# Optimization experiments

Measured on AMD Instinct MI355X. Metric: run time of the kernel, lower is better.

## Reference

```python
import jax, jax.numpy as jnp
import numpy as np
import math


def setup_inputs() -> dict:
    B, L, D, P, V = 4, 4096, 512, 128, 8
    key = jax.random.key(0)
    ki = iter(jax.random.split(key, 40))
    def rn(shape, s=0.02):
        return jax.random.normal(next(ki), shape, jnp.float32) * s
    z = lambda *s: jnp.zeros(s, jnp.float32)
    return dict(
        x=jax.random.normal(next(ki), (B, L, D), jnp.float32),
        W_omega=rn((D, D)), b_omega=z(D),
        omega_scale=jnp.full((D,), 0.01, jnp.float32),
        W_pi1=rn((D, D)), b_pi1=z(D), W_pi2=rn((D, D)), b_pi2=z(D),
        W_m1v=rn((D, D)), b_m1v=z(D),
        W_m1o=rn((D, D)), b_m1o=z(D),
        W_mag=rn((D, D)), b_mag=z(D),
        mag_scale=jnp.asarray(5.0, jnp.float32),
        W_qoff=rn((D, D)), b_qoff=z(D),
        W_kenc=rn((D, P)), b_kenc=z(P),
        W_venc=rn((D, V)), b_venc=z(V),
        W_sk1=rn((2 * D, D)), b_sk1=z(D),
        W_sk2=rn((D, P)), b_sk2=z(P),
        W_sg=rn((D, 1)), b_sg=z(1),
        W_kvo=rn((V, D)), b_kvo=z(D),
        ln_g=jnp.ones((4 * D,), jnp.float32), ln_b=z(4 * D),
        W_o1=rn((4 * D, 2 * D)), b_o1=z(2 * D),
        W_o2=rn((2 * D, D)), b_o2=z(D),
    )


def _lin(h, W, b):
    return h @ W + b


def _gelu(h):
    return jax.nn.gelu(h, approximate=False)  # torch nn.GELU default (erf)


def _forward(x, W_omega, b_omega, omega_scale, W_pi1, b_pi1, W_pi2, b_pi2,
             W_m1v, b_m1v, W_m1o, b_m1o, W_mag, b_mag, mag_scale,
             W_qoff, b_qoff, W_kenc, b_kenc, W_venc, b_venc,
             W_sk1, b_sk1, W_sk2, b_sk2, W_sg, b_sg, W_kvo, b_kvo,
             ln_g, ln_b, W_o1, b_o1, W_o2, b_o2):
    B, L, D = x.shape
    P = W_kenc.shape[1]
    # --- evolving phases ---
    omega_scaled = _lin(x, W_omega, b_omega) * jnp.abs(omega_scale)
    phi_init = _lin(_gelu(_lin(x, W_pi1, b_pi1)), W_pi2, b_pi2)
    phi = phi_init + jnp.cumsum(omega_scaled, axis=1)
    cos_phi, sin_phi = jnp.cos(phi), jnp.sin(phi)
    # --- memory 1: positional phasor memory ---
    v1 = _lin(x, W_m1v, b_m1v)
    magnitude = jax.nn.sigmoid(_lin(x, W_mag, b_mag)) * jnp.abs(mag_scale)
    wv1 = magnitude * v1
    sqrt_mag = jnp.sqrt(jnp.cumsum(magnitude, axis=1) + 1e-8)
    mem1_cos = jnp.cumsum(wv1 * cos_phi, axis=1) / sqrt_mag
    mem1_sin = jnp.cumsum(wv1 * sin_phi, axis=1) / sqrt_mag
    phi_q = phi + _lin(x, W_qoff, b_qoff)
    pos_ret = (mem1_cos * jnp.cos(phi_q) + mem1_sin * jnp.sin(phi_q)) / math.sqrt(D)
    pos_out = _lin(pos_ret, W_m1o, b_m1o)
    # --- memory 2: key/value phasor binding ---
    query_phase = jnp.tanh(_lin(x, W_kenc, b_kenc)) * math.pi
    values = _lin(x, W_venc, b_venc)                      # [B,L,V]
    store_gate = jax.nn.sigmoid(_lin(x, W_sg, b_sg))      # [B,L,1]
    positions = jnp.arange(1, L + 1, dtype=x.dtype)[None, :, None]
    context_avg = jnp.cumsum(x, axis=1) / positions
    sk_in = jnp.concatenate([x, context_avg], axis=-1)
    storage_phase = jnp.tanh(_lin(_gelu(_lin(sk_in, W_sk1, b_sk1)), W_sk2, b_sk2)) * math.pi
    store_cos, store_sin = jnp.cos(storage_phase), jnp.sin(storage_phase)  # [B,L,P]
    gv = values * store_gate                               # [B,L,V]
    # [B,L,P,V] outer products, cumsum along L
    kv_mem_cos = jnp.cumsum(store_cos[..., None] * gv[:, :, None, :], axis=1)
    kv_mem_sin = jnp.cumsum(store_sin[..., None] * gv[:, :, None, :], axis=1)
    gate_cum = jnp.clip(jnp.cumsum(store_gate, axis=1), 1.0, None)  # [B,L,1]
    inv_norm = (1.0 / jnp.sqrt(gate_cum))[..., None]
    kv_mem_cos = kv_mem_cos * inv_norm
    kv_mem_sin = kv_mem_sin * inv_norm
    q_cos, q_sin = jnp.cos(query_phase), jnp.sin(query_phase)
    kv_retrieved = (jnp.einsum('blp,blpv->blv', q_cos, kv_mem_cos)
                    + jnp.einsum('blp,blpv->blv', q_sin, kv_mem_sin)) / math.sqrt(P)
    kv_out = _lin(kv_retrieved, W_kvo, b_kvo)
    # --- output projection ---
    combined = jnp.concatenate([pos_out, kv_out, x * cos_phi, x * sin_phi], axis=-1)
    mu = combined.mean(axis=-1, keepdims=True)
    var = combined.var(axis=-1, keepdims=True)
    h = (combined - mu) / jnp.sqrt(var + 1e-5) * ln_g + ln_b
    h = _gelu(_lin(h, W_o1, b_o1))  # dropout is identity in eval mode
    return x + _lin(h, W_o2, b_o2)


def reference(x, W_omega, b_omega, omega_scale, W_pi1, b_pi1, W_pi2, b_pi2,
              W_m1v, b_m1v, W_m1o, b_m1o, W_mag, b_mag, mag_scale,
              W_qoff, b_qoff, W_kenc, b_kenc, W_venc, b_venc,
              W_sk1, b_sk1, W_sk2, b_sk2, W_sg, b_sg, W_kvo, b_kvo,
              ln_g, ln_b, W_o1, b_o1, W_o2, b_o2):
    return _forward(x, W_omega, b_omega, omega_scale, W_pi1, b_pi1, W_pi2, b_pi2,
                    W_m1v, b_m1v, W_m1o, b_m1o, W_mag, b_mag, mag_scale,
                    W_qoff, b_qoff, W_kenc, b_kenc, W_venc, b_venc,
                    W_sk1, b_sk1, W_sk2, b_sk2, W_sg, b_sg, W_kvo, b_kvo,
                    ln_g, ln_b, W_o1, b_o1, W_o2, b_o2)
```

## Files before the change

kernel.cpp:

```cpp
#include <hip/hip_runtime.h>
#include <math.h>

#define B_ 4
#define L_ 4096
#define D_ 512
#define P_ 128
#define V_ 8
#define N_ (B_*L_)
#define NC 64
#define CL (L_/NC)
#define LD ((size_t)L_*D_)
#define PI_F 3.14159265358979323846f

typedef unsigned short ushort;
typedef __attribute__((ext_vector_type(8))) short bh8;
typedef __attribute__((ext_vector_type(4))) float f4;
typedef const __attribute__((address_space(1))) unsigned int gu32;
typedef __attribute__((address_space(3))) unsigned int lu32;

__device__ __forceinline__ float geluf(float v){
    return 0.5f*v*(1.0f+erff(v*0.7071067811865475f));
}
__device__ __forceinline__ float tanhf_fast(float x){
    return 1.0f - 2.0f/(__expf(2.0f*x)+1.0f);
}
__device__ __forceinline__ ushort f2b(float f){
    union { float f; unsigned u; } v; v.f = f;
    unsigned r = (v.u + 0x7fffu + ((v.u >> 16) & 1u)) >> 16;
    return (ushort)r;
}
__device__ __forceinline__ float b2f(ushort h){
    union { unsigned u; float f; } v; v.u = ((unsigned)h) << 16;
    return v.f;
}
__device__ __forceinline__ void gload16(const ushort* g, ushort* l){
    __builtin_amdgcn_global_load_lds((gu32*)g, (lu32*)l, 16, 0, 0);
}
__device__ __forceinline__ int xcd_swz(int orig, int nwg){
    int q8 = nwg >> 3, r8 = nwg & 7;
    int xcd = orig & 7, sub = orig >> 3;
    return (xcd < r8 ? xcd*(q8+1) : r8*(q8+1) + (xcd-r8)*q8) + sub;
}

template<int ACT>
__global__ __launch_bounds__(256, 2)
void bgemm_k(const ushort* __restrict__ A, int lda,
             const ushort* __restrict__ Wt, const float* __restrict__ bias,
             ushort* __restrict__ Ob0, float* __restrict__ Of,
             int ldc, int K, int M, const float* __restrict__ addbuf)
{
    __shared__ ushort lA[2][128*32];
    __shared__ ushort lB[2][128*32];
    const int tid = threadIdx.x, lane = tid & 63, w = tid >> 6;
    const int wr = w >> 1, wc = w & 1;
    const int nbx = gridDim.x;
    const int wg = xcd_swz(blockIdx.y*nbx + blockIdx.x, nbx*gridDim.y);
    const int row0 = (wg / nbx) * 128, col0 = (wg % nbx) * 128;

    const int srow = w*32 + (lane >> 2);
    const int scol = (lane & 3) * 8;
    const ushort* gA0 = A  + (size_t)(row0 + srow)      * lda + scol;
    const ushort* gA1 = A  + (size_t)(row0 + srow + 16) * lda + scol;
    const ushort* gB0 = Wt + (size_t)(col0 + srow)      * K   + scol;
    const ushort* gB1 = Wt + (size_t)(col0 + srow + 16) * K   + scol;
    const int d0 = srow*32 + scol, d1 = (srow+16)*32 + scol;

    f4 zero4 = {0.f,0.f,0.f,0.f};
    f4 acc[4][4];
    #pragma unroll
    for (int i=0;i<4;i++)
        #pragma unroll
        for (int j=0;j<4;j++) acc[i][j] = zero4;

    const int fr = lane & 15, fq = (lane >> 4) * 8;
    gload16(gA0, &lA[0][d0]); gload16(gA1, &lA[0][d1]);
    gload16(gB0, &lB[0][d0]); gload16(gB1, &lB[0][d1]);
    __syncthreads();
    int cur = 0;
    for (int kt = 0; kt < K; kt += 32) {
        int nxt = cur ^ 1;
        if (kt + 32 < K) {
            gload16(gA0 + kt + 32, &lA[nxt][d0]); gload16(gA1 + kt + 32, &lA[nxt][d1]);
            gload16(gB0 + kt + 32, &lB[nxt][d0]); gload16(gB1 + kt + 32, &lB[nxt][d1]);
        }
        bh8 af[4], bfr[4];
        #pragma unroll
        for (int i=0;i<4;i++){
            af[i]  = *(const bh8*)&lA[cur][(wr*64 + i*16 + fr)*32 + fq];
            bfr[i] = *(const bh8*)&lB[cur][(wc*64 + i*16 + fr)*32 + fq];
        }
        #pragma unroll
        for (int i=0;i<4;i++)
            #pragma unroll
            for (int j=0;j<4;j++)
                acc[i][j] = __builtin_amdgcn_mfma_f32_16x16x32_bf16(af[i], bfr[j], acc[i][j], 0, 0, 0);
        __syncthreads();
        cur = nxt;
    }

    #pragma unroll
    for (int i=0;i<4;i++){
        int rr = row0 + wr*64 + i*16 + ((lane >> 4) << 2);
        #pragma unroll
        for (int j=0;j<4;j++){
            int cc = col0 + wc*64 + j*16 + (lane & 15);
            float bv = bias[cc];
            #pragma unroll
            for (int q=0;q<4;q++){
                int r = rr + q;
                float t = acc[i][j][q] + bv;
                if (ACT==1) t = geluf(t);
                if (addbuf) t += addbuf[(size_t)r*512 + cc];
                if (Of) Of[(size_t)r*ldc + cc] = t;
                else    Ob0[(size_t)r*ldc + cc] = f2b(t);
            }
        }
    }
}

__global__ __launch_bounds__(256, 2)
void fgemm_k(const ushort* __restrict__ A, int lda, const ushort* __restrict__ Wt,
             const float* __restrict__ bs0, const float* __restrict__ bs1,
             const float* __restrict__ bs2, const float* __restrict__ bs3,
             const float* __restrict__ bs4, const float* __restrict__ bs5,
             ushort* __restrict__ o0, ushort* __restrict__ o1p, ushort* __restrict__ o2p,
             ushort* __restrict__ o3p, ushort* __restrict__ o4p,
             ushort* __restrict__ Qc, ushort* __restrict__ Qs,
             const float* __restrict__ omsc, const float* __restrict__ magscp, int K)
{
    __shared__ ushort lA[2][128*32];
    __shared__ ushort lB[2][128*32];
    const int tid = threadIdx.x, lane = tid & 63, w = tid >> 6;
    const int wr = w >> 1, wc = w & 1;
    const int nbx = gridDim.x;
    const int wg = xcd_swz(blockIdx.y*nbx + blockIdx.x, nbx*gridDim.y);
    const int row0 = (wg / nbx) * 128, col0 = (wg % nbx) * 128;

    const int srow = w*32 + (lane >> 2);
    const int scol = (lane & 3) * 8;
    const ushort* gA0 = A  + (size_t)(row0 + srow)      * lda + scol;
    const ushort* gA1 = A  + (size_t)(row0 + srow + 16) * lda + scol;
    const ushort* gB0 = Wt + (size_t)(col0 + srow)      * K   + scol;
    const ushort* gB1 = Wt + (size_t)(col0 + srow + 16) * K   + scol;
    const int d0 = srow*32 + scol, d1 = (srow+16)*32 + scol;

    f4 zero4 = {0.f,0.f,0.f,0.f};
    f4 acc[4][4];
    #pragma unroll
    for (int i=0;i<4;i++)
        #pragma unroll
        for (int j=0;j<4;j++) acc[i][j] = zero4;

    const int fr = lane & 15, fq = (lane >> 4) * 8;
    gload16(gA0, &lA[0][d0]); gload16(gA1, &lA[0][d1]);
    gload16(gB0, &lB[0][d0]); gload16(gB1, &lB[0][d1]);
    __syncthreads();
    int cur = 0;
    for (int kt = 0; kt < K; kt += 32) {
        int nxt = cur ^ 1;
        if (kt + 32 < K) {
            gload16(gA0 + kt + 32, &lA[nxt][d0]); gload16(gA1 + kt + 32, &lA[nxt][d1]);
            gload16(gB0 + kt + 32, &lB[nxt][d0]); gload16(gB1 + kt + 32, &lB[nxt][d1]);
        }
        bh8 af[4], bfr[4];
        #pragma unroll
        for (int i=0;i<4;i++){
            af[i]  = *(const bh8*)&lA[cur][(wr*64 + i*16 + fr)*32 + fq];
            bfr[i] = *(const bh8*)&lB[cur][(wc*64 + i*16 + fr)*32 + fq];
        }
        #pragma unroll
        for (int i=0;i<4;i++)
            #pragma unroll
            for (int j=0;j<4;j++)
                acc[i][j] = __builtin_amdgcn_mfma_f32_16x16x32_bf16(af[i], bfr[j], acc[i][j], 0, 0, 0);
        __syncthreads();
        cur = nxt;
    }

    const int seg = col0 >> 9;
    if (seg == 5) {
        #pragma unroll
        for (int i=0;i<4;i++){
            int rr = row0 + wr*64 + i*16 + ((lane >> 4) << 2);
            #pragma unroll
            for (int j=0;j<4;j++){
                int lcc = (col0 - 2560) + wc*64 + j*16 + (lane & 15);
                float bv = bs5[lcc];
                #pragma unroll
                for (int q=0;q<4;q++){
                    int r = rr + q;
                    float ph = tanhf_fast(acc[i][j][q] + bv)*PI_F;
                    Qc[(size_t)r*128 + lcc] = f2b(__cosf(ph));
                    Qs[(size_t)r*128 + lcc] = f2b(__sinf(ph));
                }
            }
        }
        return;
    }
    const float* bias = seg==0?bs0: seg==1?bs1: seg==2?bs2: seg==3?bs3: bs4;
    ushort* dst = seg==0?o0: seg==1?o1p: seg==2?o2p: seg==3?o3p: o4p;
    float msc = fabsf(*magscp);
    #pragma unroll
    for (int i=0;i<4;i++){
        int rr = row0 + wr*64 + i*16 + ((lane >> 4) << 2);
        #pragma unroll
        for (int j=0;j<4;j++){
            int cc = col0 + wc*64 + j*16 + (lane & 15);
            int lcc = cc & 511;
            float bv = bias[lcc];
            float csc = (seg==0) ? fabsf(omsc[lcc]) : 1.0f;
            #pragma unroll
            for (int q=0;q<4;q++){
                int r = rr + q;
                float t = acc[i][j][q] + bv;
                if (seg==1)      t = msc/(1.0f+__expf(-t));
                else if (seg==3) t = geluf(t);
                else             t *= csc;
                dst[(size_t)r*512 + lcc] = f2b(t);
            }
        }
    }
}

__global__ __launch_bounds__(256, 2)
void mgemm_k(const ushort* __restrict__ Apos, const ushort* __restrict__ Ask,
             const ushort* __restrict__ Wm1o, const ushort* __restrict__ Wsk2,
             const float* __restrict__ bm1o, const float* __restrict__ bsk2,
             ushort* __restrict__ planes, ushort* __restrict__ Kc, ushort* __restrict__ Ks)
{
    __shared__ ushort lA[2][128*32];
    __shared__ ushort lB[2][128*32];
    const int tid = threadIdx.x, lane = tid & 63, w = tid >> 6;
    const int wr = w >> 1, wc = w & 1;
    const int nbx = gridDim.x;
    const int wg = xcd_swz(blockIdx.y*nbx + blockIdx.x, nbx*gridDim.y);
    const int row0 = (wg / nbx) * 128, col0 = (wg % nbx) * 128;
    const int seg = col0 >> 9;
    const ushort* A  = seg ? Ask  : Apos;
    const ushort* Wt = seg ? Wsk2 : Wm1o;
    const int wcol0 = seg ? (col0 - 512) : col0;
    const int K = 512;

    const int srow = w*32 + (lane >> 2);
    const int scol = (lane & 3) * 8;
    const ushort* gA0 = A  + (size_t)(row0 + srow)       * 512 + scol;
    const ushort* gA1 = A  + (size_t)(row0 + srow + 16)  * 512 + scol;
    const ushort* gB0 = Wt + (size_t)(wcol0 + srow)      * 512 + scol;
    const ushort* gB1 = Wt + (size_t)(wcol0 + srow + 16) * 512 + scol;
    const int d0 = srow*32 + scol, d1 = (srow+16)*32 + scol;

    f4 zero4 = {0.f,0.f,0.f,0.f};
    f4 acc[4][4];
    #pragma unroll
    for (int i=0;i<4;i++)
        #pragma unroll
        for (int j=0;j<4;j++) acc[i][j] = zero4;

    const int fr = lane & 15, fq = (lane >> 4) * 8;
    gload16(gA0, &lA[0][d0]); gload16(gA1, &lA[0][d1]);
    gload16(gB0, &lB[0][d0]); gload16(gB1, &lB[0][d1]);
    __syncthreads();
    int cur = 0;
    for (int kt = 0; kt < K; kt += 32) {
        int nxt = cur ^ 1;
        if (kt + 32 < K) {
            gload16(gA0 + kt + 32, &lA[nxt][d0]); gload16(gA1 + kt + 32, &lA[nxt][d1]);
            gload16(gB0 + kt + 32, &lB[nxt][d0]); gload16(gB1 + kt + 32, &lB[nxt][d1]);
        }
        bh8 af[4], bfr[4];
        #pragma unroll
        for (int i=0;i<4;i++){
            af[i]  = *(const bh8*)&lA[cur][(wr*64 + i*16 + fr)*32 + fq];
            bfr[i] = *(const bh8*)&lB[cur][(wc*64 + i*16 + fr)*32 + fq];
        }
        #pragma unroll
        for (int i=0;i<4;i++)
            #pragma unroll
            for (int j=0;j<4;j++)
                acc[i][j] = __builtin_amdgcn_mfma_f32_16x16x32_bf16(af[i], bfr[j], acc[i][j], 0, 0, 0);
        __syncthreads();
        cur = nxt;
    }

    #pragma unroll
    for (int i=0;i<4;i++){
        int rr = row0 + wr*64 + i*16 + ((lane >> 4) << 2);
        #pragma unroll
        for (int j=0;j<4;j++){
            int cc = col0 + wc*64 + j*16 + (lane & 15);
            #pragma unroll
            for (int q=0;q<4;q++){
                int r = rr + q;
                if (seg == 0){
                    planes[(size_t)r*2048 + cc] = f2b(acc[i][j][q] + bm1o[cc]);
                } else {
                    int lcc = cc - 512;
                    float ph = tanhf_fast(acc[i][j][q] + bsk2[lcc])*PI_F;
                    Kc[(size_t)r*128 + lcc] = f2b(__cosf(ph));
                    Ks[(size_t)r*128 + lcc] = f2b(__sinf(ph));
                }
            }
        }
    }
}

__global__ __launch_bounds__(256)
void wtrans_k(const float* __restrict__ W, ushort* __restrict__ Wt, int K, int M)
{
    __shared__ float tile[32][33];
    int kb = blockIdx.y*32, mb = blockIdx.x*32;
    int tx = threadIdx.x & 31, ty = threadIdx.x >> 5;
    #pragma unroll
    for (int i = ty; i < 32; i += 8)
        tile[i][tx] = W[(size_t)(kb+i)*M + mb+tx];
    __syncthreads();
    #pragma unroll
    for (int i = ty; i < 32; i += 8)
        Wt[(size_t)(mb+i)*K + kb+tx] = f2b(tile[tx][i]);
}

__global__ __launch_bounds__(256)
void fconv_k(const float* __restrict__ in, ushort* __restrict__ xctx)
{
    size_t i = ((size_t)blockIdx.x*256 + threadIdx.x) * 4;
    size_t row = i >> 9; int d = (int)(i & 511);
    float4 v = *(const float4*)(in + i);
    ushort* o = xctx + row*1024 + d;
    o[0]=f2b(v.x); o[1]=f2b(v.y); o[2]=f2b(v.z); o[3]=f2b(v.w);
}

__global__ __launch_bounds__(256)
void s1a_k(const ushort* __restrict__ omega, const float* __restrict__ xg,
           float* __restrict__ csA, float* __restrict__ csX)
{
    int bid = blockIdx.x;
    int b = bid >> 7; int rem = bid & 127;
    int dg = rem & 1, c = rem >> 1;
    int d = dg*256 + threadIdx.x;
    size_t base = ((size_t)b*L_ + (size_t)c*CL)*D_ + d;
    float sA=0.f, sX=0.f;
    for (int l=0;l<CL;l++){
        sA += b2f(omega[base + (size_t)l*D_]);
        sX += xg[base + (size_t)l*D_];
    }
    size_t ci = ((size_t)b*NC + c)*D_ + d;
    csA[ci]=sA; csX[ci]=sX;
}

__global__ __launch_bounds__(256)
void aux1_k(float* __restrict__ csA, float* __restrict__ csX,
            const float* __restrict__ sgate, float* __restrict__ rinv, int nb2)
{
    __shared__ float wsum[4];
    __shared__ float carry;
    int bb = blockIdx.x, t = threadIdx.x;
    if (bb < nb2){
        int tt = bb*256 + t;
        int b = tt >> 9, d = tt & 511;
        float* bufs[2] = {csA, csX};
        #pragma unroll
        for (int i=0;i<2;i++){
            float* p = bufs[i] + ((size_t)b*NC)*D_ + d;
            float run=0.f;
            for (int c=0;c<NC;c++){
                float v = p[(size_t)c*D_];
                p[(size_t)c*D_] = run;
                run += v;
            }
        }
        return;
    }
    int b = bb - nb2;
    int lane = t & 63, wave = t >> 6;
    if (t == 0) carry = 0.f;
    __syncthreads();
    for (int s = 0; s < L_/256; s++){
        float v = sgate[(size_t)b*L_ + s*256 + t];
        float sc = v;
        #pragma unroll
        for (int off=1; off<64; off<<=1){
            float u = __shfl_up(sc, off, 64);
            if (lane >= off) sc += u;
        }
        if (lane == 63) wsum[wave] = sc;
        __syncthreads();
        float woff = carry;
        for (int w2 = 0; w2 < wave; w2++) woff += wsum[w2];
        float inc = sc + woff;
        rinv[(size_t)b*L_ + s*256 + t] = rsqrtf(fmaxf(inc, 1.0f));
        __syncthreads();
        if (t == 255) carry = inc;
        __syncthreads();
    }
}

__global__ void prefix_k(float* a, float* b2v, float* c3, int nbuf)
{
    int t = blockIdx.x*blockDim.x + threadIdx.x;
    int b = t >> 9, d = t & 511;
    float* bufs[3] = {a,b2v,c3};
    for (int i=0;i<nbuf;i++){
        float* p = bufs[i] + ((size_t)b*NC)*D_ + d;
        float run=0.f;
        for (int c=0;c<NC;c++){
            float v = p[(size_t)c*D_];
            p[(size_t)c*D_] = run;
            run += v;
        }
    }
}

__global__ __launch_bounds__(256)
void s1c_k(const ushort* __restrict__ omega, const float* __restrict__ xg,
           const ushort* __restrict__ phi_init,
           const ushort* __restrict__ magn, const ushort* __restrict__ v1,
           const float* __restrict__ csA, const float* __restrict__ csX,
           ushort* __restrict__ cphi, ushort* __restrict__ sphi, ushort* __restrict__ xctx,
           float* __restrict__ csM, float* __restrict__ csC, float* __restrict__ csS)
{
    int bid = blockIdx.x;
    int b = bid >> 7; int rem = bid & 127;
    int dg = rem & 1, c = rem >> 1;
    int d = dg*256 + threadIdx.x;
    size_t ci = ((size_t)b*NC + c)*D_ + d;
    float phiacc = csA[ci], xacc = csX[ci];
    float sM=0.f,sC=0.f,sS=0.f;
    size_t xrow = (size_t)b*L_ + (size_t)c*CL;
    size_t base = xrow*D_ + d;
    for (int l=0;l<CL;l++){
        size_t idx = base + (size_t)l*D_;
        phiacc += b2f(omega[idx]);
        float ph = b2f(phi_init[idx]) + phiacc;
        float spv = __sinf(ph), cpv = __cosf(ph);
        cphi[idx] = f2b(cpv); sphi[idx] = f2b(spv);
        xacc += xg[idx];
        xctx[(xrow + l)*1024 + 512 + d] = f2b(__fdividef(xacc, (float)(c*CL + l + 1)));
        float m = b2f(magn[idx]); sM += m;
        float wv = m * b2f(v1[idx]);
        sC = fmaf(wv, cpv, sC); sS = fmaf(wv, spv, sS);
    }
    csM[ci]=sM; csC[ci]=sC; csS[ci]=sS;
}

__global__ __launch_bounds__(256)
void s1e_k(const ushort* __restrict__ magn, const ushort* __restrict__ v1,
           const ushort* qoff, const ushort* __restrict__ cphi, const ushort* __restrict__ sphi,
           const float* __restrict__ csM, const float* __restrict__ csC,
           const float* __restrict__ csS, ushort* pos_ret)
{
    int bid = blockIdx.x;
    int b = bid >> 7; int rem = bid & 127;
    int dg = rem & 1, c = rem >> 1;
    int d = dg*256 + threadIdx.x;
    size_t ci = ((size_t)b*NC + c)*D_ + d;
    float mA=csM[ci], cA=csC[ci], sA=csS[ci];
    size_t base = ((size_t)b*L_ + (size_t)c*CL)*D_ + d;
    for (int l=0;l<CL;l++){
        size_t idx = base + (size_t)l*D_;
        float m = b2f(magn[idx]); mA += m;
        float wv = m * b2f(v1[idx]);
        float cp = b2f(cphi[idx]), sp = b2f(sphi[idx]);
        cA = fmaf(wv, cp, cA); sA = fmaf(wv, sp, sA);
        float rs = rsqrtf(mA + 1e-8f);
        float qo = b2f(qoff[idx]);
        float sq = __sinf(qo), cq = __cosf(qo);
        float cosq = cp*cq - sp*sq;
        float sinq = sp*cq + cp*sq;
        pos_ret[idx] = f2b((cA*cosq + sA*sinq) * rs * 0.04419417382415922f);
    }
}

__global__ __launch_bounds__(256)
void vencsg_k(const float* __restrict__ xg, const float* __restrict__ Wv,
              const float* __restrict__ bv, const float* __restrict__ Wg,
              const float* __restrict__ bg,
              ushort* __restrict__ gvb, float* __restrict__ sgate)
{
    int gw = (int)((blockIdx.x*(size_t)blockDim.x + threadIdx.x) >> 6);
    int lane = threadIdx.x & 63;
    const float* xr = xg + (size_t)gw*D_;
    float pv[8] = {0,0,0,0,0,0,0,0}; float pg = 0.f;
    #pragma unroll
    for (int j=0;j<8;j++){
        int k = lane + 64*j;
        float xv = xr[k];
        #pragma unroll
        for (int v=0;v<8;v++) pv[v] = fmaf(xv, Wv[k*8+v], pv[v]);
        pg = fmaf(xv, Wg[k], pg);
    }
    #pragma unroll
    for (int off=32; off>0; off>>=1){
        #pragma unroll
        for (int v=0;v<8;v++) pv[v] += __shfl_down(pv[v], off, 64);
        pg += __shfl_down(pg, off, 64);
    }
    if (lane==0){
        float sg = 1.0f/(1.0f+__expf(-(pg + bg[0])));
        #pragma unroll
        for (int v=0;v<8;v++) gvb[(size_t)gw*8+v] = f2b((pv[v] + bv[v]) * sg);
        sgate[gw] = sg;
    }
}

__global__ __launch_bounds__(256)
void kvsum_k(const ushort* __restrict__ Kc, const ushort* __restrict__ Ks,
             const ushort* __restrict__ gvb, float* __restrict__ csKV)
{
    int bid = blockIdx.x;
    int b = bid >> 6, c = bid & 63;
    int t = threadIdx.x; int p = t & 127; int v0 = (t>>7)*4;
    size_t row0 = (size_t)b*L_ + (size_t)c*64;
    float ac[4]={0,0,0,0}, as[4]={0,0,0,0};
    for (int l=0;l<64;l++){
        size_t r = row0 + l;
        float kc = b2f(Kc[r*(size_t)P_ + p]);
        float ks = b2f(Ks[r*(size_t)P_ + p]);
        #pragma unroll
        for (int j=0;j<4;j++){
            float gv = b2f(gvb[r*(size_t)V_ + v0 + j]);
            ac[j] = fmaf(kc, gv, ac[j]);
            as[j] = fmaf(ks, gv, as[j]);
        }
    }
    float* base = csKV + ((size_t)b*64 + c)*2048;
    #pragma unroll
    for (int j=0;j<4;j++){
        base[p*V_ + v0 + j] = ac[j];
        base[1024 + p*V_ + v0 + j] = as[j];
    }
}

__global__ void kvpfx_k(float* __restrict__ csKV)
{
    int t = blockIdx.x*blockDim.x + threadIdx.x;
    int b = t >> 11, si = t & 2047;
    float* ptr = csKV + ((size_t)b*64)*2048 + si;
    float run=0.f;
    for (int c=0;c<64;c++){
        float v = ptr[(size_t)c*2048];
        ptr[(size_t)c*2048] = run;
        run += v;
    }
}

__global__ __launch_bounds__(256)
void kv2_k(const ushort* __restrict__ Qc, const ushort* __restrict__ Qs,
           const ushort* __restrict__ Kc, const ushort* __restrict__ Ks,
           const ushort* __restrict__ gvb, const float* __restrict__ rinv,
           const float* __restrict__ csKV, float* __restrict__ kvret)
{
    __shared__ ushort sS[64][66];
    __shared__ float sM[2048];
    __shared__ float sgv[64][8];
    int tile = blockIdx.x, b = blockIdx.y;
    int t = threadIdx.x, lane = t & 63, w = t >> 6;
    int wr = w >> 1, wc = w & 1;
    size_t row0 = (size_t)b*L_ + (size_t)tile*64;
    const float* kvb = csKV + ((size_t)b*64 + tile)*2048;
    #pragma unroll
    for (int k=0;k<8;k++) sM[t + k*256] = kvb[t + k*256];
    #pragma unroll
    for (int k=0;k<2;k++){
        int idx = t + k*256; int l = idx >> 3, v = idx & 7;
        sgv[l][v] = b2f(gvb[(row0 + l)*(size_t)V_ + v]);
    }
    f4 zero4 = {0.f,0.f,0.f,0.f};
    f4 acc[2][2];
    #pragma unroll
    for (int i=0;i<2;i++)
        #pragma unroll
        for (int j=0;j<2;j++) acc[i][j] = zero4;
    #pragma unroll
    for (int ks=0; ks<8; ks++){
        const ushort* Ab = (ks<4) ? Qc : Qs;
        const ushort* Bb = (ks<4) ? Kc : Ks;
        int kb = (ks&3)*32 + (lane>>4)*8;
        bh8 af[2], bfr[2];
        #pragma unroll
        for (int i=0;i<2;i++)
            af[i] = *(const bh8*)(Ab + (row0 + wr*32 + i*16 + (lane&15))*(size_t)P_ + kb);
        #pragma unroll
        for (int j=0;j<2;j++)
            bfr[j] = *(const bh8*)(Bb + (row0 + wc*32 + j*16 + (lane&15))*(size_t)P_ + kb);
        #pragma unroll
        for (int i=0;i<2;i++)
            #pragma unroll
            for (int j=0;j<2;j++)
                acc[i][j] = __builtin_amdgcn_mfma_f32_16x16x32_bf16(af[i], bfr[j], acc[i][j], 0, 0, 0);
    }
    #pragma unroll
    for (int i=0;i<2;i++){
        #pragma unroll
        for (int j=0;j<2;j++){
            int cc = wc*32 + j*16 + (lane & 15);
            #pragma unroll
            for (int q=0;q<4;q++){
                int lr = wr*32 + i*16 + ((lane>>4)<<2) + q;
                sS[lr][cc] = f2b((cc <= lr) ? acc[i][j][q] : 0.f);
            }
        }
    }
    __syncthreads();
    int l = t & 63, vh = t >> 6; int v0 = vh*2;
    const ushort* qcr = Qc + (row0 + l)*(size_t)P_;
    const ushort* qsr = Qs + (row0 + l)*(size_t)P_;
    float a0=0.f, a1=0.f;
    #pragma unroll
    for (int pc=0; pc<16; pc++){
        bh8 qc8 = *(const bh8*)(qcr + pc*8);
        bh8 qs8 = *(const bh8*)(qsr + pc*8);
        #pragma unroll
        for (int e=0;e<8;e++){
            int p = pc*8+e;
            float qc = b2f((ushort)qc8[e]), qs = b2f((ushort)qs8[e]);
            a0 += qc*sM[p*8+v0]   + qs*sM[1024+p*8+v0];
            a1 += qc*sM[p*8+v0+1] + qs*sM[1024+p*8+v0+1];
        }
    }
    for (int c=0;c<64;c++){
        float sv = b2f(sS[l][c]);
        a0 = fmaf(sv, sgv[c][v0],   a0);
        a1 = fmaf(sv, sgv[c][v0+1], a1);
    }
    float rn = rinv[row0 + l] * 0.08838834764831845f;
    kvret[(row0+l)*(size_t)V_ + v0]   = a0*rn;
    kvret[(row0+l)*(size_t)V_ + v0+1] = a1*rn;
}

__global__ __launch_bounds__(256)
void kvo_k(const float* __restrict__ kvret, const float* __restrict__ Wkvo,
           const float* __restrict__ bkvo, ushort* __restrict__ pl)
{
    size_t idx = (size_t)blockIdx.x*256 + threadIdx.x;
    size_t n = idx >> 9; int d = (int)(idx & 511);
    float s = bkvo[d];
    #pragma unroll
    for (int v=0;v<8;v++) s = fmaf(kvret[n*8+v], Wkvo[v*512 + d], s);
    pl[n*2048 + 512 + d] = f2b(s);
}

__global__ __launch_bounds__(256)
void cmb_k(const float* __restrict__ xg, const ushort* __restrict__ cphi,
           const ushort* __restrict__ sphi,
           const float* __restrict__ ln_g, const float* __restrict__ ln_b,
           ushort* pl)
{
    __shared__ float red[8];
    int n = blockIdx.x; int t = threadIdx.x;
    int wave = t>>6, lane = t&63;
    float v_[8]; float sum=0.f, sumsq=0.f;
    #pragma unroll
    for (int i=0;i<8;i++){
        int cidx = t + i*256;
        int seg = cidx >> 9, cc = cidx & 511;
        float v;
        if (seg <= 1) v = b2f(pl[(size_t)n*2048 + cidx]);
        else {
            size_t id = (size_t)n*D_ + cc;
            v = xg[id] * b2f((seg==2) ? cphi[id] : sphi[id]);
        }
        v_[i]=v; sum += v; sumsq = fmaf(v,v,sumsq);
    }
    #pragma unroll
    for (int off=32; off>0; off>>=1){
        sum += __shfl_xor(sum, off, 64);
        sumsq += __shfl_xor(sumsq, off, 64);
    }
    if (lane==0){ red[wave]=sum; red[wave+4]=sumsq; }
    __syncthreads();
    float s = red[0]+red[1]+red[2]+red[3];
    float q = red[4]+red[5]+red[6]+red[7];
    float mu = s * (1.0f/2048.0f);
    float var = q * (1.0f/2048.0f) - mu*mu;
    float rstd = rsqrtf(var + 1e-5f);
    #pragma unroll
    for (int i=0;i<8;i++){
        int cidx = t + i*256;
        float h = (v_[i]-mu)*rstd*ln_g[cidx] + ln_b[cidx];
        pl[(size_t)n*2048 + cidx] = f2b(h);
    }
}

__global__ void copyx_k(const float* __restrict__ x, float* __restrict__ out, size_t n)
{
    size_t i = (size_t)blockIdx.x*256 + threadIdx.x;
    if (i < n) out[i] = x[i];
}

struct WS {
    ushort *wt_fused,*wt_pi2,*wt_sk1,*wt_sk2,*wt_m1o,*wt_o1,*wt_o2;
    ushort *xctx, *pool;
    ushort *Qc,*Qs,*Kc,*Ks,*gvb,*cphi,*sphi;
    float *sgate,*rinv,*kvret;
    float *csA,*csX,*csM,*csC,*csS,*csKV;
};

static size_t ws_layout(WS& w, char* base, int NB)
{
    size_t off = 0;
    auto al = [&](size_t bytes)->char* {
        char* p = base + off; off = (off + bytes + 255) & ~(size_t)255; return p;
    };
    size_t R = (size_t)NB * L_;
    w.wt_fused=(ushort*)al((size_t)2688*512*2);
    w.wt_pi2 =(ushort*)al(512*512*2);
    w.wt_sk1 =(ushort*)al((size_t)512*1024*2); w.wt_sk2=(ushort*)al(128*512*2);
    w.wt_m1o =(ushort*)al(512*512*2);
    w.wt_o1  =(ushort*)al((size_t)1024*2048*2); w.wt_o2=(ushort*)al((size_t)512*1024*2);
    w.xctx=(ushort*)al(R*1024*2);
    w.pool=(ushort*)al(R*512*2*6);
    w.Qc=(ushort*)al(R*128*2); w.Qs=(ushort*)al(R*128*2);
    w.Kc=(ushort*)al(R*128*2); w.Ks=(ushort*)al(R*128*2);
    w.gvb=(ushort*)al(R*8*2);
    w.cphi=(ushort*)al(R*512*2); w.sphi=(ushort*)al(R*512*2);
    w.sgate=(float*)al(R*4); w.rinv=(float*)al(R*4); w.kvret=(float*)al(R*8*4);
    w.csA=(float*)al((size_t)NB*NC*512*4); w.csX=(float*)al((size_t)NB*NC*512*4);
    w.csM=(float*)al((size_t)NB*NC*512*4); w.csC=(float*)al((size_t)NB*NC*512*4);
    w.csS=(float*)al((size_t)NB*NC*512*4);
    w.csKV=(float*)al((size_t)NB*64*2048*4);
    return off;
}

extern "C" void kernel_launch(void* const* d_in, const int* in_sizes, int n_in,
                              void* d_out, int out_size, void* d_ws, size_t ws_size,
                              hipStream_t stream)
{
    const float* x        =(const float*)d_in[0];
    const float* W_omega  =(const float*)d_in[1];  const float* b_omega=(const float*)d_in[2];
    const float* omega_sc =(const float*)d_in[3];
    const float* W_pi1    =(const float*)d_in[4];  const float* b_pi1 =(const float*)d_in[5];
    const float* W_pi2    =(const float*)d_in[6];  const float* b_pi2 =(const float*)d_in[7];
    const float* W_m1v    =(const float*)d_in[8];  const float* b_m1v =(const float*)d_in[9];
    const float* W_m1o    =(const float*)d_in[10]; const float* b_m1o =(const float*)d_in[11];
    const float* W_mag    =(const float*)d_in[12]; const float* b_mag =(const float*)d_in[13];
    const float* mag_sc   =(const float*)d_in[14];
    const float* W_qoff   =(const float*)d_in[15]; const float* b_qoff=(const float*)d_in[16];
    const float* W_kenc   =(const float*)d_in[17]; const float* b_kenc=(const float*)d_in[18];
    const float* W_venc   =(const float*)d_in[19]; const float* b_venc=(const float*)d_in[20];
    const float* W_sk1    =(const float*)d_in[21]; const float* b_sk1 =(const float*)d_in[22];
    const float* W_sk2    =(const float*)d_in[23]; const float* b_sk2 =(const float*)d_in[24];
    const float* W_sg     =(const float*)d_in[25]; const float* b_sg  =(const float*)d_in[26];
    const float* W_kvo    =(const float*)d_in[27]; const float* b_kvo =(const float*)d_in[28];
    const float* ln_g     =(const float*)d_in[29]; const float* ln_b  =(const float*)d_in[30];
    const float* W_o1     =(const float*)d_in[31]; const float* b_o1  =(const float*)d_in[32];
    const float* W_o2     =(const float*)d_in[33]; const float* b_o2  =(const float*)d_in[34];
    float* out = (float*)d_out;

    char* wsb = (char*)d_ws;
    WS w;
    int NB = 4;
    if (ws_layout(w, wsb, 4) > ws_size) {
        NB = 2;
        if (ws_layout(w, wsb, 2) > ws_size) {
            NB = 1;
            if (ws_layout(w, wsb, 1) > ws_size) {
                copyx_k<<<dim3((unsigned)(((size_t)N_*D_ + 255)/256)), dim3(256), 0, stream>>>(x, out, (size_t)N_*D_);
                return;
            }
        }
    }

    dim3 blk(256);
    auto wt = [&](const float* W, ushort* Wt, int K, int M){
        wtrans_k<<<dim3(M/32, K/32), blk, 0, stream>>>(W, Wt, K, M);
    };
    wt(W_omega, w.wt_fused + (size_t)0*512*512, 512, 512);
    wt(W_mag,   w.wt_fused + (size_t)1*512*512, 512, 512);
    wt(W_m1v,   w.wt_fused + (size_t)2*512*512, 512, 512);
    wt(W_pi1,   w.wt_fused + (size_t)3*512*512, 512, 512);
    wt(W_qoff,  w.wt_fused + (size_t)4*512*512, 512, 512);
    wt(W_kenc,  w.wt_fused + (size_t)5*512*512, 512, 128);
    wt(W_pi2,w.wt_pi2,512,512);
    wt(W_sk1,w.wt_sk1,1024,512);  wt(W_sk2,w.wt_sk2,512,128);
    wt(W_m1o,w.wt_m1o,512,512);
    wt(W_o1,w.wt_o1,2048,1024);   wt(W_o2,w.wt_o2,1024,512);

    const int R = NB * L_;
    const size_t SL = (size_t)R * 512;
    ushort* bA = w.pool;        ushort* bB = w.pool + SL;
    ushort* bC = w.pool + 2*SL; ushort* bD = w.pool + 3*SL;
    ushort* bE = w.pool + 4*SL; ushort* bF = w.pool + 5*SL;
    ushort* planes = w.pool;
    ushort* h1 = w.pool + 4*SL;

    #define GEMM(ACT,A,lda,Wt_,bias_,Ob0_,Of_,ldc,K_,M_,add_) \
        bgemm_k<ACT><<<dim3((M_)/128, R/128), blk, 0, stream>>>(A,lda,Wt_,bias_,Ob0_,Of_,ldc,K_,M_,add_)

    for (int g = 0; g < B_/NB; ++g) {
        const float* xg = x + (size_t)g*NB*LD;
        float* outg = out + (size_t)g*NB*LD;

        fconv_k<<<dim3((unsigned)((size_t)R*512/1024)), blk, 0, stream>>>(xg, w.xctx);

        fgemm_k<<<dim3(2688/128, R/128), blk, 0, stream>>>(
            w.xctx,1024, w.wt_fused, b_omega,b_mag,b_m1v,b_pi1,b_qoff,b_kenc,
            bA,bB,bC,bD,bF, w.Qc,w.Qs, omega_sc, mag_sc, 512);
        GEMM(0, bD,512, w.wt_pi2, b_pi2, bE,(float*)0, 512, 512,512, (const float*)0);
        vencsg_k<<<dim3((unsigned)((size_t)R*64/256)), blk, 0, stream>>>(xg, W_venc,b_venc, W_sg,b_sg, w.gvb, w.sgate);
        s1a_k<<<dim3(NB*NC*2), blk, 0, stream>>>(bA, xg, w.csA, w.csX);
        aux1_k<<<dim3(NB*2 + NB), blk, 0, stream>>>(w.csA, w.csX, w.sgate, w.rinv, NB*2);
        s1c_k<<<dim3(NB*NC*2), blk, 0, stream>>>(bA, xg, bE, bB, bC, w.csA, w.csX,
                                                 w.cphi, w.sphi, w.xctx, w.csM, w.csC, w.csS);
        prefix_k<<<dim3(NB*2), blk, 0, stream>>>(w.csM, w.csC, w.csS, 3);
        s1e_k<<<dim3(NB*NC*2), blk, 0, stream>>>(bB, bC, bF, w.cphi, w.sphi,
                                                 w.csM, w.csC, w.csS, bF);

        GEMM(1, w.xctx,1024, w.wt_sk1, b_sk1, bD,(float*)0, 512, 1024,512, (const float*)0);
        mgemm_k<<<dim3(640/128, R/128), blk, 0, stream>>>(
            bF, bD, w.wt_m1o, w.wt_sk2, b_m1o, b_sk2, planes, w.Kc, w.Ks);

        kvsum_k<<<dim3(NB*64), blk, 0, stream>>>(w.Kc, w.Ks, w.gvb, w.csKV);
        kvpfx_k<<<dim3(NB*8), blk, 0, stream>>>(w.csKV);
        kv2_k<<<dim3(64, NB), blk, 0, stream>>>(w.Qc, w.Qs, w.Kc, w.Ks, w.gvb, w.rinv, w.csKV, w.kvret);
        kvo_k<<<dim3((unsigned)((size_t)R*512/256)), blk, 0, stream>>>(w.kvret, W_kvo, b_kvo, planes);

        cmb_k<<<dim3(R), blk, 0, stream>>>(xg, w.cphi, w.sphi, ln_g, ln_b, planes);
        GEMM(1, planes,2048, w.wt_o1, b_o1, h1,(float*)0, 1024, 2048,1024, (const float*)0);
        GEMM(0, h1,1024, w.wt_o2, b_o2, (ushort*)0,outg, 512, 1024,512, xg);
    }
    #undef GEMM
}
```

Before: 541.0 us.

## Replace generic GEMM with 256x128 tile, K=64 swizzled-LDS pipelined kernel

Swaps the 128x128, K-step-32 bf16 GEMM for a 512-thread kernel that computes 256x128 output tiles with a K-step of 64. LDS is XOR-swizzled to avoid bank conflicts, and global-to-LDS loads are overlapped with explicit vmcnt waits and raw s_barrier. The larger tile and deeper K step are meant to raise arithmetic intensity and cut barrier overhead per MFMA. In exchange it uses more LDS, allows one block per CU, and launches fewer workgroups.

```diff
diff --git a/kernel.cpp b/kernel.cpp
--- a/kernel.cpp
+++ b/kernel.cpp
@@ -43,27 +43,25 @@
 }
 
 template<int ACT>
-__global__ __launch_bounds__(256, 2)
-void bgemm_k(const ushort* __restrict__ A, int lda,
+__global__ __launch_bounds__(512, 1)
+void cgemm_k(const ushort* __restrict__ A, int lda,
              const ushort* __restrict__ Wt, const float* __restrict__ bias,
-             ushort* __restrict__ Ob0, float* __restrict__ Of,
-             int ldc, int K, int M, const float* __restrict__ addbuf)
-{
-    __shared__ ushort lA[2][128*32];
-    __shared__ ushort lB[2][128*32];
+             ushort* __restrict__ Ob, float* __restrict__ Of,
+             int ldc, int K, const float* __restrict__ addbuf)
+{
+    __shared__ ushort lA[2][256*64];
+    __shared__ ushort lB[2][128*64];
     const int tid = threadIdx.x, lane = tid & 63, w = tid >> 6;
     const int wr = w >> 1, wc = w & 1;
     const int nbx = gridDim.x;
     const int wg = xcd_swz(blockIdx.y*nbx + blockIdx.x, nbx*gridDim.y);
-    const int row0 = (wg / nbx) * 128, col0 = (wg % nbx) * 128;
-
-    const int srow = w*32 + (lane >> 2);
-    const int scol = (lane & 3) * 8;
-    const ushort* gA0 = A  + (size_t)(row0 + srow)      * lda + scol;
-    const ushort* gA1 = A  + (size_t)(row0 + srow + 16) * lda + scol;
-    const ushort* gB0 = Wt + (size_t)(col0 + srow)      * K   + scol;
-    const ushort* gB1 = Wt + (size_t)(col0 + srow + 16) * K   + scol;
-    const int d0 = srow*32 + scol, d1 = (srow+16)*32 + scol;
+    const int row0 = (wg / nbx) * 256, col0 = (wg % nbx) * 128;
+
+    const int sr = tid >> 3, scp = tid & 7;
+    const int scsrc = (scp ^ (sr & 7)) * 8;
+    const ushort* gA = A  + (size_t)(row0 + sr) * lda + scsrc;
+    const ushort* gB = Wt + (size_t)(col0 + sr) * K   + scsrc;
+    const int dof = sr*64 + scp*8;
 
     f4 zero4 = {0.f,0.f,0.f,0.f};
     f4 acc[4][4];
@@ -72,30 +70,50 @@
         #pragma unroll
         for (int j=0;j<4;j++) acc[i][j] = zero4;
 
-    const int fr = lane & 15, fq = (lane >> 4) * 8;
-    gload16(gA0, &lA[0][d0]); gload16(gA1, &lA[0][d1]);
-    gload16(gB0, &lB[0][d0]); gload16(gB1, &lB[0][d1]);
-    __syncthreads();
-    int cur = 0;
-    for (int kt = 0; kt < K; kt += 32) {
-        int nxt = cur ^ 1;
-        if (kt + 32 < K) {
-            gload16(gA0 + kt + 32, &lA[nxt][d0]); gload16(gA1 + kt + 32, &lA[nxt][d1]);
-            gload16(gB0 + kt + 32, &lB[nxt][d0]); gload16(gB1 + kt + 32, &lB[nxt][d1]);
-        }
-        bh8 af[4], bfr[4];
-        #pragma unroll
-        for (int i=0;i<4;i++){
-            af[i]  = *(const bh8*)&lA[cur][(wr*64 + i*16 + fr)*32 + fq];
-            bfr[i] = *(const bh8*)&lB[cur][(wc*64 + i*16 + fr)*32 + fq];
-        }
-        #pragma unroll
-        for (int i=0;i<4;i++)
-            #pragma unroll
-            for (int j=0;j<4;j++)
-                acc[i][j] = __builtin_amdgcn_mfma_f32_16x16x32_bf16(af[i], bfr[j], acc[i][j], 0, 0, 0);
-        __syncthreads();
-        cur = nxt;
+    auto stage = [&](int buf, int kt){
+        #pragma unroll
+        for (int is=0; is<4; ++is)
+            gload16(gA + (size_t)is*64*lda + kt, &lA[buf][is*64*64 + dof]);
+        #pragma unroll
+        for (int is=0; is<2; ++is)
+            gload16(gB + (size_t)is*64*K + kt, &lB[buf][is*64*64 + dof]);
+    };
+
+    const int NT = K >> 6;
+    stage(0, 0);
+    for (int t2=0; t2<NT; ++t2){
+        int cur = t2 & 1;
+        if (t2+1 < NT){
+            stage(cur^1, (t2+1)<<6);
+            asm volatile("s_waitcnt vmcnt(6)" ::: "memory");
+        } else {
+            asm volatile("s_waitcnt vmcnt(0)" ::: "memory");
+        }
+        __builtin_amdgcn_s_barrier();
+        __builtin_amdgcn_sched_barrier(0);
+        #pragma unroll
+        for (int h=0; h<2; ++h){
+            bh8 af[4], bf_[4];
+            #pragma unroll
+            for (int i=0;i<4;i++){
+                int row = wr*64 + i*16 + (lane & 15);
+                int pc = (h*4 + (lane >> 4)) ^ (row & 7);
+                af[i] = *(const bh8*)&lA[cur][row*64 + pc*8];
+            }
+            #pragma unroll
+            for (int j=0;j<4;j++){
+                int row = wc*64 + j*16 + (lane & 15);
+                int pc = (h*4 + (lane >> 4)) ^ (row & 7);
+                bf_[j] = *(const bh8*)&lB[cur][row*64 + pc*8];
+            }
+            #pragma unroll
+            for (int i=0;i<4;i++)
+                #pragma unroll
+                for (int j=0;j<4;j++)
+                    acc[i][j] = __builtin_amdgcn_mfma_f32_16x16x32_bf16(af[i], bf_[j], acc[i][j], 0, 0, 0);
+        }
+        __builtin_amdgcn_sched_barrier(0);
+        __builtin_amdgcn_s_barrier();
     }
 
     #pragma unroll
@@ -109,10 +127,13 @@
             for (int q=0;q<4;q++){
                 int r = rr + q;
                 float t = acc[i][j][q] + bv;
-                if (ACT==1) t = geluf(t);
-                if (addbuf) t += addbuf[(size_t)r*512 + cc];
-                if (Of) Of[(size_t)r*ldc + cc] = t;
-                else    Ob0[(size_t)r*ldc + cc] = f2b(t);
+                if (ACT==2){
+                    if (addbuf) t += addbuf[(size_t)r*512 + cc];
+                    Of[(size_t)r*ldc + cc] = t;
+                } else {
+                    if (ACT==1) t = geluf(t);
+                    Ob[(size_t)r*ldc + cc] = f2b(t);
+                }
             }
         }
     }
@@ -783,8 +804,8 @@
     ushort* planes = w.pool;
     ushort* h1 = w.pool + 4*SL;
 
-    #define GEMM(ACT,A,lda,Wt_,bias_,Ob0_,Of_,ldc,K_,M_,add_) \
-        bgemm_k<ACT><<<dim3((M_)/128, R/128), blk, 0, stream>>>(A,lda,Wt_,bias_,Ob0_,Of_,ldc,K_,M_,add_)
+    #define CGEMM(ACT,A,lda,Wt_,bias_,Ob_,Of_,ldc,K_,M_,add_) \
+        cgemm_k<ACT><<<dim3((M_)/128, R/256), dim3(512), 0, stream>>>(A,lda,Wt_,bias_,Ob_,Of_,ldc,K_,add_)
 
     for (int g = 0; g < B_/NB; ++g) {
         const float* xg = x + (size_t)g*NB*LD;
@@ -795,7 +816,7 @@
         fgemm_k<<<dim3(2688/128, R/128), blk, 0, stream>>>(
             w.xctx,1024, w.wt_fused, b_omega,b_mag,b_m1v,b_pi1,b_qoff,b_kenc,
             bA,bB,bC,bD,bF, w.Qc,w.Qs, omega_sc, mag_sc, 512);
-        GEMM(0, bD,512, w.wt_pi2, b_pi2, bE,(float*)0, 512, 512,512, (const float*)0);
+        CGEMM(0, bD,512, w.wt_pi2, b_pi2, bE,(float*)0, 512, 512,512, (const float*)0);
         vencsg_k<<<dim3((unsigned)((size_t)R*64/256)), blk, 0, stream>>>(xg, W_venc,b_venc, W_sg,b_sg, w.gvb, w.sgate);
         s1a_k<<<dim3(NB*NC*2), blk, 0, stream>>>(bA, xg, w.csA, w.csX);
         aux1_k<<<dim3(NB*2 + NB), blk, 0, stream>>>(w.csA, w.csX, w.sgate, w.rinv, NB*2);
@@ -805,7 +826,7 @@
         s1e_k<<<dim3(NB*NC*2), blk, 0, stream>>>(bB, bC, bF, w.cphi, w.sphi,
                                                  w.csM, w.csC, w.csS, bF);
 
-        GEMM(1, w.xctx,1024, w.wt_sk1, b_sk1, bD,(float*)0, 512, 1024,512, (const float*)0);
+        CGEMM(1, w.xctx,1024, w.wt_sk1, b_sk1, bD,(float*)0, 512, 1024,512, (const float*)0);
         mgemm_k<<<dim3(640/128, R/128), blk, 0, stream>>>(
             bF, bD, w.wt_m1o, w.wt_sk2, b_m1o, b_sk2, planes, w.Kc, w.Ks);
 
@@ -815,8 +836,8 @@
         kvo_k<<<dim3((unsigned)((size_t)R*512/256)), blk, 0, stream>>>(w.kvret, W_kvo, b_kvo, planes);
 
         cmb_k<<<dim3(R), blk, 0, stream>>>(xg, w.cphi, w.sphi, ln_g, ln_b, planes);
-        GEMM(1, planes,2048, w.wt_o1, b_o1, h1,(float*)0, 1024, 2048,1024, (const float*)0);
-        GEMM(0, h1,1024, w.wt_o2, b_o2, (ushort*)0,outg, 512, 1024,512, xg);
-    }
-    #undef GEMM
-}
+        CGEMM(1, planes,2048, w.wt_o1, b_o1, h1,(float*)0, 1024, 2048,1024, (const float*)0);
+        CGEMM(2, h1,1024, w.wt_o2, b_o2, (ushort*)0,outg, 512, 1024,512, xg);
+    }
+    #undef CGEMM
+}
```

New measurement: 546.4 us. No clear change (+1.0%).
